# Kernel optimization log

Hardware: AMD Instinct MI355X
Metric: run time of the kernel (lower is better)

## Reference

```python
import jax, jax.numpy as jnp
import numpy as np

BATCH = 131072
N = 64          # total bits
PARTS = 16      # len(partition) == dpp_size
M = 4           # bits per part
D = PARTS
EPS = 1e-8


def _colnorm(a):
    return a / jnp.linalg.norm(a, axis=0, keepdims=True)


def setup_inputs() -> dict:
    key = jax.random.key(0)
    k0, k1, k2, k3, k4 = jax.random.split(key, 5)
    x = jax.random.randint(k0, (BATCH, N), 0, 2, dtype=jnp.int32)
    W = jax.random.normal(k1, (PARTS, (1 << M) - 1), dtype=jnp.float32)
    A = _colnorm(jax.random.normal(k2, (D, D), dtype=jnp.float32))
    B = _colnorm(jax.random.normal(k3, (D, D), dtype=jnp.float32))
    C = _colnorm(jax.random.normal(k4, (D, D), dtype=jnp.float32))
    return {"x": x, "W": W, "A": A, "B": B, "C": C}


def reference(x, W, A, B, C):
    batch = x.shape[0]
    # --- Simple PCs (vectorized over the 16 parts): bit-pack each 4-bit part ---
    bits = x.reshape(batch, PARTS, M)                       # contiguous partition
    pow2 = (1 << jnp.arange(M)).astype(jnp.int32)           # [M]
    idx = jnp.sum(bits * pow2, axis=-1)                     # [B, P] in [0, 2^M)
    w = jax.nn.softmax(W, axis=-1)                          # [P, 2^M - 1]
    w = jnp.concatenate([jnp.zeros((PARTS, 1), w.dtype), w], axis=-1)  # [P, 2^M]
    p = w[jnp.arange(PARTS)[None, :], idx]                  # [B, P]

    # --- L matrix: sym PD part + skew part ---
    I = jnp.eye(D, dtype=A.dtype)
    L0 = A.T @ A + (B @ C.T - C @ B.T) + EPS * I            # [D, D]

    # column-scale by p, then force diagonal to 1 where p == 0
    Lp = L0[None, :, :] * p[:, None, :]                     # [B, D, D]
    eye_b = jnp.eye(D, dtype=bool)
    mask = eye_b[None, :, :] & (p == 0.0)[:, :, None]
    Lp = jnp.where(mask, jnp.asarray(1.0, Lp.dtype), Lp)

    sign, logabs = jnp.linalg.slogdet(Lp)                   # [B]
    y = logabs + jnp.log(jax.lax.stop_gradient(sign))       # nan if det < 0 (matches torch.logdet)
    s0, la0 = jnp.linalg.slogdet(L0 + I)
    alpha = la0 + jnp.log(jax.lax.stop_gradient(s0))
    return y - alpha
```

## Files before the change

kernel.cpp:

```cpp
#include <hip/hip_runtime.h>
#include <math.h>

#define BATCH 131072
#define EPS 1e-8f


__global__ __launch_bounds__(64, 1) void stageA_kernel(const float* __restrict__ W,
                                                       const float* __restrict__ A,
                                                       const float* __restrict__ Bm,
                                                       const float* __restrict__ Cm,
                                                       float* __restrict__ ws) {
    __shared__ float sL0[256];
    int lt = threadIdx.x;
    #pragma unroll
    for (int q = 0; q < 4; ++q) {
        int e = lt * 4 + q;
        int i = e >> 4, j = e & 15;
        float s = 0.f;
        #pragma unroll
        for (int k = 0; k < 16; ++k) {
            s += A[k * 16 + i] * A[k * 16 + j];
            s += Bm[i * 16 + k] * Cm[j * 16 + k]
               - Cm[i * 16 + k] * Bm[j * 16 + k];
        }
        if (i == j) s += EPS;
        sL0[e] = s;
    }
    __syncthreads();

    unsigned tg = blockIdx.x * 64u + (unsigned)lt;

    if (tg >= 288u && tg < 304u) {
        int r = (int)tg - 288;
        float row[15];
        float mx = -1e30f;
        #pragma unroll
        for (int q = 0; q < 15; ++q) { row[q] = W[r * 15 + q]; mx = fmaxf(mx, row[q]); }
        float se = 0.f;
        #pragma unroll
        for (int q = 0; q < 15; ++q) se += expf(row[q] - mx);
        float lse = mx + logf(se);
        ws[r * 16 + 0] = 0.f;
        #pragma unroll
        for (int q = 0; q < 15; ++q) ws[r * 16 + 1 + q] = row[q] - lse;
    }

    if (tg > 256u) return;
    bool isAlpha = (tg == 256u);
    unsigned h = isAlpha ? 0xFFu : tg;

    float a[16][16];
    #pragma unroll
    for (int r = 0; r < 16; ++r) {
        int i = (r < 8) ? (8 + r) : (r - 8);
        bool pi = (i < 8) ? true : (((h >> (i - 8)) & 1u) != 0u);
        #pragma unroll
        for (int c = 0; c < 16; ++c) {
            int j = (c < 8) ? (8 + c) : (c - 8);
            bool pj = (j < 8) ? true : (((h >> (j - 8)) & 1u) != 0u);
            float v = (pi && pj) ? sL0[i * 16 + j] : ((r == c) ? 1.f : 0.f);
            if (isAlpha && r == c) v += 1.f;
            a[r][c] = v;
        }
    }

    float plog = 0.f;
    #pragma unroll
    for (int k = 0; k < 8; ++k) {
        float piv = a[k][k];
        plog += __logf(fabsf(piv));
        float inv = 1.0f / piv;
        #pragma unroll
        for (int r2 = k + 1; r2 < 16; ++r2) {
            float f = a[r2][k] * inv;
            #pragma unroll
            for (int c2 = k + 1; c2 < 16; ++c2)
                a[r2][c2] = fmaf(-f, a[k][c2], a[r2][c2]);
        }
    }

    if (!isAlpha) {
        #pragma unroll
        for (int i = 0; i < 8; ++i)
            #pragma unroll
            for (int j = 0; j < 8; ++j)
                ws[512 + h * 64 + i * 8 + j] = a[8 + i][8 + j];
        ws[17408 + h] = plog;
    } else {
        #pragma unroll
        for (int k = 8; k < 16; ++k) {
            float piv = a[k][k];
            plog += __logf(fabsf(piv));
            float inv = 1.0f / piv;
            #pragma unroll
            for (int r2 = k + 1; r2 < 16; ++r2) {
                float f = a[r2][k] * inv;
                #pragma unroll
                for (int c2 = k + 1; c2 < 16; ++c2)
                    a[r2][c2] = fmaf(-f, a[k][c2], a[r2][c2]);
            }
        }
        ws[256] = plog;
    }
}

__global__ __launch_bounds__(256) void main_kernel(const int4* __restrict__ x,
                                                   const float* __restrict__ ws,
                                                   float* __restrict__ out) {
    __shared__ float slw[256];
    __shared__ float sAlpha;
    int lt = threadIdx.x;
    slw[lt] = ws[lt];
    if (lt == 0) sAlpha = ws[256];
    __syncthreads();

    int g = blockIdx.x * 256 + lt;
    const int4* xb = x + (size_t)g * 16;

    float lw = 0.f;
    unsigned mask = 0;
    #pragma unroll
    for (int j = 0; j < 16; ++j) {
        int4 v = xb[j];
        int idx = v.x + 2 * v.y + 4 * v.z + 8 * v.w;
        lw += slw[j * 16 + idx];
        mask |= (idx != 0 ? 1u : 0u) << j;
    }
    const unsigned h2 = mask >> 8;
    const unsigned lo = mask & 255u;

    const float4* S4 = (const float4*)(ws + 512 + (size_t)h2 * 64);
    float a[8][8];
    #pragma unroll
    for (int i = 0; i < 16; ++i) {
        const float4 q4 = S4[i];
        const int ri = i >> 1, cb = (i & 1) * 4;
        a[ri][cb + 0] = q4.x; a[ri][cb + 1] = q4.y;
        a[ri][cb + 2] = q4.z; a[ri][cb + 3] = q4.w;
    }
    #pragma unroll
    for (int i = 0; i < 8; ++i) {
        const bool bi = ((lo >> i) & 1u) != 0u;
        #pragma unroll
        for (int j = 0; j < 8; ++j) {
            const bool bj = ((lo >> j) & 1u) != 0u;
            if (!(bi && bj)) a[i][j] = (i == j) ? 1.f : 0.f;
        }
    }

    float ld = ws[17408 + h2] + lw - sAlpha;
    #pragma unroll
    for (int k = 0; k < 8; ++k) {
        const float piv = a[k][k];
        ld += __logf(fabsf(piv));
        const float inv = 1.0f / piv;
        #pragma unroll
        for (int i = k + 1; i < 8; ++i) {
            const float f = a[i][k] * inv;
            #pragma unroll
            for (int j = k + 1; j < 8; ++j)
                a[i][j] = fmaf(-f, a[k][j], a[i][j]);
        }
    }
    out[g] = ld;
}

extern "C" void kernel_launch(void* const* d_in, const int* in_sizes, int n_in,
                              void* d_out, int out_size, void* d_ws, size_t ws_size,
                              hipStream_t stream) {
    const float* W = (const float*)d_in[1];
    const float* A = (const float*)d_in[2];
    const float* B = (const float*)d_in[3];
    const float* C = (const float*)d_in[4];
    const int4*  x = (const int4*)d_in[0];
    float* ws  = (float*)d_ws;
    float* out = (float*)d_out;

    stageA_kernel<<<5, 64, 0, stream>>>(W, A, B, C, ws);
    main_kernel<<<BATCH / 256, 256, 0, stream>>>(x, ws, out);
}
```

Measured before the change: 90.49 us.

## Coalesce x loads across wave and reduce per-sample results with shuffles

Each wave now loads its 64 samples' input cooperatively, so consecutive lanes read consecutive int4s instead of each thread striding through its own 256-byte row. Per-part log weights are summed with 16-lane xor shuffles and the nonzero masks are built with a wave ballot, then redistributed so each lane owns one sample. It transposes the shared log-weight table to match the new access pattern. This adds shuffle and ballot work per step and changes the sample-to-lane mapping, which alters the output write order.

Measured after the change: 90.38 us. No clear change (-0.1%).

```diff
diff --git a/kernel.cpp b/kernel.cpp
--- a/kernel.cpp
+++ b/kernel.cpp
@@ -107,27 +107,45 @@
 __global__ __launch_bounds__(256) void main_kernel(const int4* __restrict__ x,
                                                    const float* __restrict__ ws,
                                                    float* __restrict__ out) {
-    __shared__ float slw[256];
+    __shared__ float slwT[256];
     __shared__ float sAlpha;
     int lt = threadIdx.x;
-    slw[lt] = ws[lt];
+    {
+        float v = ws[lt];
+        slwT[(lt & 15) * 16 + (lt >> 4)] = v;
+    }
     if (lt == 0) sAlpha = ws[256];
     __syncthreads();
 
-    int g = blockIdx.x * 256 + lt;
-    const int4* xb = x + (size_t)g * 16;
+    const int lane = lt & 63;
+    const int waveInBlk = lt >> 6;
+    const int sampleBase = blockIdx.x * 256 + waveInBlk * 64;
+    const int4* xw = x + (size_t)sampleBase * 16;
 
-    float lw = 0.f;
-    unsigned mask = 0;
+    const int p  = lane & 15;
+    const int gq = lane >> 4;
+
+    float lwKeep = 0.f;
+    unsigned maskKeep = 0u;
     #pragma unroll
-    for (int j = 0; j < 16; ++j) {
-        int4 v = xb[j];
+    for (int step = 0; step < 16; ++step) {
+        int4 v = xw[step * 64 + lane];
         int idx = v.x + 2 * v.y + 4 * v.z + 8 * v.w;
-        lw += slw[j * 16 + idx];
-        mask |= (idx != 0 ? 1u : 0u) << j;
+        float c = slwT[idx * 16 + p];
+        unsigned long long bal = __ballot(idx != 0);
+        c += __shfl_xor(c, 1, 16);
+        c += __shfl_xor(c, 2, 16);
+        c += __shfl_xor(c, 4, 16);
+        c += __shfl_xor(c, 8, 16);
+        if (p == step) {
+            lwKeep   = c;
+            maskKeep = (unsigned)((bal >> (gq * 16)) & 0xFFFFull);
+        }
     }
-    const unsigned h2 = mask >> 8;
-    const unsigned lo = mask & 255u;
+
+    const int g = sampleBase + p * 4 + gq;
+    const unsigned h2 = maskKeep >> 8;
+    const unsigned lo = maskKeep & 255u;
 
     const float4* S4 = (const float4*)(ws + 512 + (size_t)h2 * 64);
     float a[8][8];
@@ -148,7 +166,7 @@
         }
     }
 
-    float ld = ws[17408 + h2] + lw - sAlpha;
+    float ld = ws[17408 + h2] + lwKeep - sAlpha;
     #pragma unroll
     for (int k = 0; k < 8; ++k) {
         const float piv = a[k][k];
```
